# Kernel tuning notes

Hardware: AMD Instinct MI355X
Metric: run time of the kernel (lower is better)

The kernel has to match this reference:

```python
import jax, jax.numpy as jnp
import numpy as np

NUM_HEADS = 6
DIM = 192
WIN = 7  # window_size = (7, 7), n = 49
N = WIN * WIN
TABLE = (2 * WIN - 1) * (2 * WIN - 1)  # 169
SCALE = (DIM // NUM_HEADS) ** (-0.5)


def setup_inputs() -> dict:
    key = jax.random.key(0)
    k1, k2, k3, k4, k5, k6 = jax.random.split(key, 6)
    B_ = 8192   # num_windows * batch = 1024 * 8
    NW = 1024   # windows per image (224/7)^2
    qkv = jax.random.normal(k1, (B_, N, 3 * DIM), dtype=jnp.float32)
    rpi = jax.random.randint(k2, (N, N), 0, TABLE, dtype=jnp.int64)
    # shift-window mask: 0 where attend, -100 where masked (Swin convention)
    mask = jnp.where(jax.random.uniform(k3, (NW, N, N)) < 0.8, 0.0, -100.0).astype(jnp.float32)
    bias_table = 0.02 * jax.random.normal(k4, (TABLE, NUM_HEADS), dtype=jnp.float32)
    proj_w = 0.02 * jax.random.normal(k5, (DIM, DIM), dtype=jnp.float32)
    proj_b = jnp.zeros((DIM,), dtype=jnp.float32)
    return {"qkv": qkv, "rpi": rpi, "mask": mask,
            "bias_table": bias_table, "proj_w": proj_w, "proj_b": proj_b}


def reference(qkv, rpi, mask, bias_table, proj_w, proj_b):
    b_, n, c3 = qkv.shape
    c = c3 // 3
    hd = c // NUM_HEADS
    # (b_, n, 3, h, hd) -> (3, b_, h, n, hd)
    qkv = qkv.reshape(b_, n, 3, NUM_HEADS, hd).transpose(2, 0, 3, 1, 4)
    q, k, v = qkv[0], qkv[1], qkv[2]
    attn = jnp.einsum('bhid,bhjd->bhij', q * SCALE, k)  # (b_, h, n, n)
    # relative position bias gather: (n*n,) -> (n, n, h) -> (h, n, n)
    rpb = bias_table[rpi.reshape(-1)].reshape(n, n, NUM_HEADS).transpose(2, 0, 1)
    attn = attn + rpb[None]
    nw = mask.shape[0]
    attn = attn.reshape(b_ // nw, nw, NUM_HEADS, n, n) + mask[None, :, None]
    attn = jax.nn.softmax(attn.reshape(b_, NUM_HEADS, n, n), axis=-1)
    x = jnp.einsum('bhij,bhjd->bhid', attn, v)          # (b_, h, n, hd)
    x = x.transpose(0, 2, 1, 3).reshape(b_, n, c)
    return x @ proj_w.T + proj_b
```

## Files before the change

### kernel.cpp

```cpp
#include <hip/hip_runtime.h>

#define NH 6
#define NTOK 49
#define CDIM 192
#define NWIN 1024
#define SCALE 0.17677669529663687f

typedef __bf16 bf16x8 __attribute__((ext_vector_type(8)));
typedef float f32x4 __attribute__((ext_vector_type(4)));
typedef unsigned short u16;
typedef unsigned int u32;

__device__ __forceinline__ u16 bfr(float x) { return __builtin_bit_cast(u16, (__bf16)x); }

__global__ void build_wb(const float* __restrict__ w, u16* __restrict__ wb) {
    int i = blockIdx.x * 256 + threadIdx.x;
    if (i < CDIM * CDIM) wb[i] = bfr(w[i]);
}

__global__ __launch_bounds__(256, 4)
void swin_fused(const float* __restrict__ qkv, const int* __restrict__ rpi,
                const float* __restrict__ mask, const float* __restrict__ bias_table,
                const u16* __restrict__ wb, const float* __restrict__ proj_b,
                float* __restrict__ out) {
    __shared__ u16 k_s[64][40];
    __shared__ u16 vT_s[32][72];
    __shared__ u16 p_s[64][72];

    const int tid = threadIdx.x;
    const int b = blockIdx.x;
    const int wn = b & (NWIN - 1);
    const int wv = tid >> 6;
    const int lane = tid & 63;
    const int lg = lane >> 4;
    const int lc = lane & 15;

    const float* qkvb = qkv + (size_t)b * (NTOK * 3 * CDIM);
    const float* mrow = mask + (size_t)wn * (NTOK * NTOK);
    const f32x4 fzero = {0.f, 0.f, 0.f, 0.f};

    const int n0 = tid >> 3, f0 = tid & 7;
    const bool s1 = tid < 136;
    const int n1 = (tid + 256) >> 3, f1 = (tid + 256) & 7;
    const float* kb0 = qkvb + n0 * 576 + CDIM + f0 * 4;
    const float* vb0 = qkvb + n0 * 576 + 2 * CDIM + f0 * 4;
    const float* kb1 = qkvb + n1 * 576 + CDIM + f1 * 4;
    const float* vb1 = qkvb + n1 * 576 + 2 * CDIM + f1 * 4;

    const int qrow = (16 * wv + lc < NTOK) ? 16 * wv + lc : NTOK - 1;
    const float* qptr = qkvb + (size_t)qrow * 576 + 8 * lg;

    float4 kp0 = *reinterpret_cast<const float4*>(kb0);
    float4 vp0 = *reinterpret_cast<const float4*>(vb0);
    float4 kp1 = {0, 0, 0, 0}, vp1 = {0, 0, 0, 0};
    if (s1) {
        kp1 = *reinterpret_cast<const float4*>(kb1);
        vp1 = *reinterpret_cast<const float4*>(vb1);
    }
    float4 qfA = *reinterpret_cast<const float4*>(qptr);
    float4 qfB = *reinterpret_cast<const float4*>(qptr + 4);

    int bofs[4][4];
    float maddf[4][4];
    {
        const int i = 16 * wv + lc;
#pragma unroll
        for (int t = 0; t < 4; ++t)
#pragma unroll
            for (int r = 0; r < 4; ++r) {
                const int j = 16 * t + 4 * lg + r;
                const bool valid = (i < NTOK) && (j < NTOK);
                const int ij = valid ? i * NTOK + j : 0;
                bofs[t][r] = rpi[ij] * NH;
                maddf[t][r] = valid ? mrow[ij] : -1e30f;
            }
    }

    for (int idx = tid; idx < 512; idx += 256) {
        const int d = idx >> 4, m = idx & 15;
        if (m) vT_s[d][48 + m] = 0;
    }
    for (int idx = tid; idx < 600; idx += 256) {
        const int rr = idx / 40, cc = idx % 40;
        k_s[49 + rr][cc] = 0;
    }

    {
        ushort4 ko;
        ko.x = bfr(kp0.x); ko.y = bfr(kp0.y); ko.z = bfr(kp0.z); ko.w = bfr(kp0.w);
        *reinterpret_cast<ushort4*>(&k_s[n0][f0 * 4]) = ko;
        const int d0 = f0 * 4;
        vT_s[d0 + 0][n0] = bfr(vp0.x); vT_s[d0 + 1][n0] = bfr(vp0.y);
        vT_s[d0 + 2][n0] = bfr(vp0.z); vT_s[d0 + 3][n0] = bfr(vp0.w);
        if (s1) {
            ushort4 k1;
            k1.x = bfr(kp1.x); k1.y = bfr(kp1.y); k1.z = bfr(kp1.z); k1.w = bfr(kp1.w);
            *reinterpret_cast<ushort4*>(&k_s[n1][f1 * 4]) = k1;
            const int d1 = f1 * 4;
            vT_s[d1 + 0][n1] = bfr(vp1.x); vT_s[d1 + 1][n1] = bfr(vp1.y);
            vT_s[d1 + 2][n1] = bfr(vp1.z); vT_s[d1 + 3][n1] = bfr(vp1.w);
        }
    }
    __syncthreads();

    bf16x8 af[NH];

#pragma unroll
    for (int h = 0; h < NH; ++h) {
        if (h + 1 < NH) {
            kp0 = *reinterpret_cast<const float4*>(kb0 + (h + 1) * 32);
            vp0 = *reinterpret_cast<const float4*>(vb0 + (h + 1) * 32);
            if (s1) {
                kp1 = *reinterpret_cast<const float4*>(kb1 + (h + 1) * 32);
                vp1 = *reinterpret_cast<const float4*>(vb1 + (h + 1) * 32);
            }
        }

        bf16x8 aq;
        aq[0] = (__bf16)(qfA.x * SCALE); aq[1] = (__bf16)(qfA.y * SCALE);
        aq[2] = (__bf16)(qfA.z * SCALE); aq[3] = (__bf16)(qfA.w * SCALE);
        aq[4] = (__bf16)(qfB.x * SCALE); aq[5] = (__bf16)(qfB.y * SCALE);
        aq[6] = (__bf16)(qfB.z * SCALE); aq[7] = (__bf16)(qfB.w * SCALE);
        if (h + 1 < NH) {
            qfA = *reinterpret_cast<const float4*>(qptr + (h + 1) * 32);
            qfB = *reinterpret_cast<const float4*>(qptr + (h + 1) * 32 + 4);
        }

        float bias_v[4][4];
#pragma unroll
        for (int t = 0; t < 4; ++t)
#pragma unroll
            for (int r = 0; r < 4; ++r)
                bias_v[t][r] = bias_table[bofs[t][r] + h];

        bf16x8 bk[4];
#pragma unroll
        for (int t = 0; t < 4; ++t)
            bk[t] = *reinterpret_cast<const bf16x8*>(&k_s[16 * t + lc][8 * lg]);
        f32x4 acc[4];
#pragma unroll
        for (int t = 0; t < 4; ++t)
            acc[t] = __builtin_amdgcn_mfma_f32_16x16x32_bf16(bk[t], aq, fzero, 0, 0, 0);

        float vals[4][4];
#pragma unroll
        for (int t = 0; t < 4; ++t)
#pragma unroll
            for (int r = 0; r < 4; ++r)
                vals[t][r] = acc[t][r] + bias_v[t][r] + maddf[t][r];

        float mx[4];
#pragma unroll
        for (int t = 0; t < 4; ++t)
            mx[t] = fmaxf(fmaxf(vals[t][0], vals[t][1]), fmaxf(vals[t][2], vals[t][3]));
        float m = fmaxf(fmaxf(mx[0], mx[1]), fmaxf(mx[2], mx[3]));
        m = fmaxf(m, __shfl_xor(m, 16));
        m = fmaxf(m, __shfl_xor(m, 32));

        float e[4][4];
        float s = 0.f;
#pragma unroll
        for (int t = 0; t < 4; ++t) {
            float st = 0.f;
#pragma unroll
            for (int r = 0; r < 4; ++r) { e[t][r] = __expf(vals[t][r] - m); st += e[t][r]; }
            s += st;
        }
        s += __shfl_xor(s, 16);
        s += __shfl_xor(s, 32);
        const float rs = 1.0f / s;

        {
            u16* prow = &p_s[16 * wv + lc][4 * lg];
#pragma unroll
            for (int t = 0; t < 4; ++t) {
                ushort4 pk;
                pk.x = bfr(e[t][0] * rs); pk.y = bfr(e[t][1] * rs);
                pk.z = bfr(e[t][2] * rs); pk.w = bfr(e[t][3] * rs);
                *reinterpret_cast<ushort4*>(prow + 16 * t) = pk;
            }
        }

        f32x4 xacc[2] = {fzero, fzero};
#pragma unroll
        for (int ks = 0; ks < 2; ++ks) {
            const bf16x8 pa = *reinterpret_cast<const bf16x8*>(&p_s[16 * wv + lc][32 * ks + 8 * lg]);
#pragma unroll
            for (int ct = 0; ct < 2; ++ct) {
                const bf16x8 vv = *reinterpret_cast<const bf16x8*>(&vT_s[16 * ct + lc][32 * ks + 8 * lg]);
                xacc[ct] = __builtin_amdgcn_mfma_f32_16x16x32_bf16(pa, vv, xacc[ct], 0, 0, 0);
            }
        }

#pragma unroll
        for (int ct = 0; ct < 2; ++ct)
#pragma unroll
            for (int r = 0; r < 4; ++r)
                p_s[16 * wv + 4 * lg + r][16 * ct + lc] = bfr(xacc[ct][r]);
        af[h] = *reinterpret_cast<const bf16x8*>(&p_s[16 * wv + lc][8 * lg]);

        if (h + 1 < NH) {
            __syncthreads();
            ushort4 ko;
            ko.x = bfr(kp0.x); ko.y = bfr(kp0.y); ko.z = bfr(kp0.z); ko.w = bfr(kp0.w);
            *reinterpret_cast<ushort4*>(&k_s[n0][f0 * 4]) = ko;
            const int d0 = f0 * 4;
            vT_s[d0 + 0][n0] = bfr(vp0.x); vT_s[d0 + 1][n0] = bfr(vp0.y);
            vT_s[d0 + 2][n0] = bfr(vp0.z); vT_s[d0 + 3][n0] = bfr(vp0.w);
            if (s1) {
                ushort4 k1;
                k1.x = bfr(kp1.x); k1.y = bfr(kp1.y); k1.z = bfr(kp1.z); k1.w = bfr(kp1.w);
                *reinterpret_cast<ushort4*>(&k_s[n1][f1 * 4]) = k1;
                const int d1 = f1 * 4;
                vT_s[d1 + 0][n1] = bfr(vp1.x); vT_s[d1 + 1][n1] = bfr(vp1.y);
                vT_s[d1 + 2][n1] = bfr(vp1.z); vT_s[d1 + 3][n1] = bfr(vp1.w);
            }
            __syncthreads();
        }
    }

    f32x4 pacc[12];
#pragma unroll
    for (int ct = 0; ct < 12; ++ct) pacc[ct] = fzero;

#pragma unroll
    for (int ks = 0; ks < NH; ++ks) {
#pragma unroll
        for (int ct = 0; ct < 12; ++ct) {
            const bf16x8 bw = *reinterpret_cast<const bf16x8*>(wb + (16 * ct + lc) * CDIM + ks * 32 + 8 * lg);
            pacc[ct] = __builtin_amdgcn_mfma_f32_16x16x32_bf16(af[ks], bw, pacc[ct], 0, 0, 0);
        }
    }

#pragma unroll
    for (int ct = 0; ct < 12; ++ct) {
        const int c = 16 * ct + lc;
        const float pb = proj_b[c];
#pragma unroll
        for (int r = 0; r < 4; ++r) {
            const int i = 16 * wv + 4 * lg + r;
            if (i < NTOK)
                out[(size_t)b * (NTOK * CDIM) + i * CDIM + c] = pacc[ct][r] + pb;
        }
    }
}

extern "C" void kernel_launch(void* const* d_in, const int* in_sizes, int n_in,
                              void* d_out, int out_size, void* d_ws, size_t ws_size,
                              hipStream_t stream) {
    const float* qkv        = (const float*)d_in[0];
    const int*   rpi        = (const int*)d_in[1];
    const float* mask       = (const float*)d_in[2];
    const float* bias_table = (const float*)d_in[3];
    const float* proj_w     = (const float*)d_in[4];
    const float* proj_b     = (const float*)d_in[5];
    float* out = (float*)d_out;
    u16* wb = (u16*)d_ws;

    const int nblk = in_sizes[0] / (NTOK * 3 * CDIM);

    build_wb<<<(CDIM * CDIM + 255) / 256, 256, 0, stream>>>(proj_w, wb);
    swin_fused<<<nblk, 256, 0, stream>>>(qkv, rpi, mask, bias_table, wb, proj_b, out);
}
```

Measured before the change: 561.4 us.

## Load K/V per wave directly from global and split projection by output columns

Each wave now reads its own K and V fragments straight from global memory into registers in MFMA layout, so the shared K/V staging buffers and the two block barriers per head go away. Per-head attention outputs go to a shared row buffer, and after one barrier each wave computes 48 output columns for all 64 rows of the projection instead of all 192 columns for its 16 rows. The cost is that every wave loads all of K and V, which is four times the global and L2 traffic for those, and the V loads are scalar strided reads that are poorly coalesced.

```diff
diff --git a/kernel.cpp b/kernel.cpp
--- a/kernel.cpp
+++ b/kernel.cpp
@@ -23,9 +23,8 @@
                 const float* __restrict__ mask, const float* __restrict__ bias_table,
                 const u16* __restrict__ wb, const float* __restrict__ proj_b,
                 float* __restrict__ out) {
-    __shared__ u16 k_s[64][40];
-    __shared__ u16 vT_s[32][72];
-    __shared__ u16 p_s[64][72];
+    __shared__ u16 xb_s[64][200];
+    __shared__ u16 p_s[4][16][72];
 
     const int tid = threadIdx.x;
     const int b = blockIdx.x;
@@ -39,24 +38,26 @@
     const float* mrow = mask + (size_t)wn * (NTOK * NTOK);
     const f32x4 fzero = {0.f, 0.f, 0.f, 0.f};
 
-    const int n0 = tid >> 3, f0 = tid & 7;
-    const bool s1 = tid < 136;
-    const int n1 = (tid + 256) >> 3, f1 = (tid + 256) & 7;
-    const float* kb0 = qkvb + n0 * 576 + CDIM + f0 * 4;
-    const float* vb0 = qkvb + n0 * 576 + 2 * CDIM + f0 * 4;
-    const float* kb1 = qkvb + n1 * 576 + CDIM + f1 * 4;
-    const float* vb1 = qkvb + n1 * 576 + 2 * CDIM + f1 * 4;
-
     const int qrow = (16 * wv + lc < NTOK) ? 16 * wv + lc : NTOK - 1;
     const float* qptr = qkvb + (size_t)qrow * 576 + 8 * lg;
-
-    float4 kp0 = *reinterpret_cast<const float4*>(kb0);
-    float4 vp0 = *reinterpret_cast<const float4*>(vb0);
-    float4 kp1 = {0, 0, 0, 0}, vp1 = {0, 0, 0, 0};
-    if (s1) {
-        kp1 = *reinterpret_cast<const float4*>(kb1);
-        vp1 = *reinterpret_cast<const float4*>(vb1);
-    }
+    const float* kptr[4];
+#pragma unroll
+    for (int t = 0; t < 4; ++t) {
+        const int krow = (16 * t + lc < NTOK) ? 16 * t + lc : NTOK - 1;
+        kptr[t] = qkvb + (size_t)krow * 576 + CDIM + 8 * lg;
+    }
+    const float* vptr[2];
+    int vrow[2][8];
+#pragma unroll
+    for (int ks = 0; ks < 2; ++ks)
+#pragma unroll
+        for (int j = 0; j < 8; ++j) {
+            const int r = 32 * ks + 8 * lg + j;
+            vrow[ks][j] = (r < NTOK ? r : NTOK - 1) * 576;
+        }
+    vptr[0] = qkvb + 2 * CDIM + lc;
+    vptr[1] = qkvb + 2 * CDIM + lc;
+
     float4 qfA = *reinterpret_cast<const float4*>(qptr);
     float4 qfB = *reinterpret_cast<const float4*>(qptr + 4);
 
@@ -76,45 +77,29 @@
             }
     }
 
-    for (int idx = tid; idx < 512; idx += 256) {
-        const int d = idx >> 4, m = idx & 15;
-        if (m) vT_s[d][48 + m] = 0;
-    }
-    for (int idx = tid; idx < 600; idx += 256) {
-        const int rr = idx / 40, cc = idx % 40;
-        k_s[49 + rr][cc] = 0;
-    }
-
-    {
-        ushort4 ko;
-        ko.x = bfr(kp0.x); ko.y = bfr(kp0.y); ko.z = bfr(kp0.z); ko.w = bfr(kp0.w);
-        *reinterpret_cast<ushort4*>(&k_s[n0][f0 * 4]) = ko;
-        const int d0 = f0 * 4;
-        vT_s[d0 + 0][n0] = bfr(vp0.x); vT_s[d0 + 1][n0] = bfr(vp0.y);
-        vT_s[d0 + 2][n0] = bfr(vp0.z); vT_s[d0 + 3][n0] = bfr(vp0.w);
-        if (s1) {
-            ushort4 k1;
-            k1.x = bfr(kp1.x); k1.y = bfr(kp1.y); k1.z = bfr(kp1.z); k1.w = bfr(kp1.w);
-            *reinterpret_cast<ushort4*>(&k_s[n1][f1 * 4]) = k1;
-            const int d1 = f1 * 4;
-            vT_s[d1 + 0][n1] = bfr(vp1.x); vT_s[d1 + 1][n1] = bfr(vp1.y);
-            vT_s[d1 + 2][n1] = bfr(vp1.z); vT_s[d1 + 3][n1] = bfr(vp1.w);
-        }
-    }
-    __syncthreads();
-
-    bf16x8 af[NH];
-
 #pragma unroll
     for (int h = 0; h < NH; ++h) {
-        if (h + 1 < NH) {
-            kp0 = *reinterpret_cast<const float4*>(kb0 + (h + 1) * 32);
-            vp0 = *reinterpret_cast<const float4*>(vb0 + (h + 1) * 32);
-            if (s1) {
-                kp1 = *reinterpret_cast<const float4*>(kb1 + (h + 1) * 32);
-                vp1 = *reinterpret_cast<const float4*>(vb1 + (h + 1) * 32);
-            }
-        }
+        float4 kfA[4], kfB[4];
+#pragma unroll
+        for (int t = 0; t < 4; ++t) {
+            kfA[t] = *reinterpret_cast<const float4*>(kptr[t] + h * 32);
+            kfB[t] = *reinterpret_cast<const float4*>(kptr[t] + h * 32 + 4);
+        }
+        float vf[2][2][8];
+#pragma unroll
+        for (int ct = 0; ct < 2; ++ct)
+#pragma unroll
+            for (int ks = 0; ks < 2; ++ks)
+#pragma unroll
+                for (int j = 0; j < 8; ++j)
+                    vf[ct][ks][j] = vptr[ks][vrow[ks][j] + h * 32 + 16 * ct];
+
+        float bias_v[4][4];
+#pragma unroll
+        for (int t = 0; t < 4; ++t)
+#pragma unroll
+            for (int r = 0; r < 4; ++r)
+                bias_v[t][r] = bias_table[bofs[t][r] + h];
 
         bf16x8 aq;
         aq[0] = (__bf16)(qfA.x * SCALE); aq[1] = (__bf16)(qfA.y * SCALE);
@@ -126,21 +111,16 @@
             qfB = *reinterpret_cast<const float4*>(qptr + (h + 1) * 32 + 4);
         }
 
-        float bias_v[4][4];
-#pragma unroll
-        for (int t = 0; t < 4; ++t)
-#pragma unroll
-            for (int r = 0; r < 4; ++r)
-                bias_v[t][r] = bias_table[bofs[t][r] + h];
-
-        bf16x8 bk[4];
-#pragma unroll
-        for (int t = 0; t < 4; ++t)
-            bk[t] = *reinterpret_cast<const bf16x8*>(&k_s[16 * t + lc][8 * lg]);
         f32x4 acc[4];
 #pragma unroll
-        for (int t = 0; t < 4; ++t)
-            acc[t] = __builtin_amdgcn_mfma_f32_16x16x32_bf16(bk[t], aq, fzero, 0, 0, 0);
+        for (int t = 0; t < 4; ++t) {
+            bf16x8 bk;
+            bk[0] = (__bf16)kfA[t].x; bk[1] = (__bf16)kfA[t].y;
+            bk[2] = (__bf16)kfA[t].z; bk[3] = (__bf16)kfA[t].w;
+            bk[4] = (__bf16)kfB[t].x; bk[5] = (__bf16)kfB[t].y;
+            bk[6] = (__bf16)kfB[t].z; bk[7] = (__bf16)kfB[t].w;
+            acc[t] = __builtin_amdgcn_mfma_f32_16x16x32_bf16(bk, aq, fzero, 0, 0, 0);
+        }
 
         float vals[4][4];
 #pragma unroll
@@ -171,7 +151,7 @@
         const float rs = 1.0f / s;
 
         {
-            u16* prow = &p_s[16 * wv + lc][4 * lg];
+            u16* prow = &p_s[wv][lc][4 * lg];
 #pragma unroll
             for (int t = 0; t < 4; ++t) {
                 ushort4 pk;
@@ -181,66 +161,67 @@
             }
         }
 
+        bf16x8 vv[2][2];
+#pragma unroll
+        for (int ct = 0; ct < 2; ++ct)
+#pragma unroll
+            for (int ks = 0; ks < 2; ++ks)
+#pragma unroll
+                for (int j = 0; j < 8; ++j)
+                    vv[ct][ks][j] = (__bf16)vf[ct][ks][j];
+
         f32x4 xacc[2] = {fzero, fzero};
 #pragma unroll
         for (int ks = 0; ks < 2; ++ks) {
-            const bf16x8 pa = *reinterpret_cast<const bf16x8*>(&p_s[16 * wv + lc][32 * ks + 8 * lg]);
-#pragma unroll
-            for (int ct = 0; ct < 2; ++ct) {
-                const bf16x8 vv = *reinterpret_cast<const bf16x8*>(&vT_s[16 * ct + lc][32 * ks + 8 * lg]);
-                xacc[ct] = __builtin_amdgcn_mfma_f32_16x16x32_bf16(pa, vv, xacc[ct], 0, 0, 0);
+            const bf16x8 pa = *reinterpret_cast<const bf16x8*>(&p_s[wv][lc][32 * ks + 8 * lg]);
+#pragma unroll
+            for (int ct = 0; ct < 2; ++ct)
+                xacc[ct] = __builtin_amdgcn_mfma_f32_16x16x32_bf16(pa, vv[ct][ks], xacc[ct], 0, 0, 0);
+        }
+
+#pragma unroll
+        for (int ct = 0; ct < 2; ++ct)
+#pragma unroll
+            for (int r = 0; r < 4; ++r)
+                xb_s[16 * wv + 4 * lg + r][32 * h + 16 * ct + lc] = bfr(xacc[ct][r]);
+    }
+
+    __syncthreads();
+
+    f32x4 pacc[3][4];
+#pragma unroll
+    for (int ct = 0; ct < 3; ++ct)
+#pragma unroll
+        for (int rt = 0; rt < 4; ++rt) pacc[ct][rt] = fzero;
+
+#pragma unroll
+    for (int ks = 0; ks < 6; ++ks) {
+        bf16x8 af[4];
+#pragma unroll
+        for (int rt = 0; rt < 4; ++rt)
+            af[rt] = *reinterpret_cast<const bf16x8*>(&xb_s[16 * rt + lc][32 * ks + 8 * lg]);
+#pragma unroll
+        for (int ct = 0; ct < 3; ++ct) {
+            const int c = 48 * wv + 16 * ct + lc;
+            const bf16x8 bw = *reinterpret_cast<const bf16x8*>(wb + c * CDIM + 32 * ks + 8 * lg);
+#pragma unroll
+            for (int rt = 0; rt < 4; ++rt)
+                pacc[ct][rt] = __builtin_amdgcn_mfma_f32_16x16x32_bf16(af[rt], bw, pacc[ct][rt], 0, 0, 0);
+        }
+    }
+
+#pragma unroll
+    for (int ct = 0; ct < 3; ++ct) {
+        const int c = 48 * wv + 16 * ct + lc;
+        const float pb = proj_b[c];
+#pragma unroll
+        for (int rt = 0; rt < 4; ++rt) {
+#pragma unroll
+            for (int r = 0; r < 4; ++r) {
+                const int i = 16 * rt + 4 * lg + r;
+                if (i < NTOK)
+                    out[(size_t)b * (NTOK * CDIM) + i * CDIM + c] = pacc[ct][rt][r] + pb;
             }
-        }
-
-#pragma unroll
-        for (int ct = 0; ct < 2; ++ct)
-#pragma unroll
-            for (int r = 0; r < 4; ++r)
-                p_s[16 * wv + 4 * lg + r][16 * ct + lc] = bfr(xacc[ct][r]);
-        af[h] = *reinterpret_cast<const bf16x8*>(&p_s[16 * wv + lc][8 * lg]);
-
-        if (h + 1 < NH) {
-            __syncthreads();
-            ushort4 ko;
-            ko.x = bfr(kp0.x); ko.y = bfr(kp0.y); ko.z = bfr(kp0.z); ko.w = bfr(kp0.w);
-            *reinterpret_cast<ushort4*>(&k_s[n0][f0 * 4]) = ko;
-            const int d0 = f0 * 4;
-            vT_s[d0 + 0][n0] = bfr(vp0.x); vT_s[d0 + 1][n0] = bfr(vp0.y);
-            vT_s[d0 + 2][n0] = bfr(vp0.z); vT_s[d0 + 3][n0] = bfr(vp0.w);
-            if (s1) {
-                ushort4 k1;
-                k1.x = bfr(kp1.x); k1.y = bfr(kp1.y); k1.z = bfr(kp1.z); k1.w = bfr(kp1.w);
-                *reinterpret_cast<ushort4*>(&k_s[n1][f1 * 4]) = k1;
-                const int d1 = f1 * 4;
-                vT_s[d1 + 0][n1] = bfr(vp1.x); vT_s[d1 + 1][n1] = bfr(vp1.y);
-                vT_s[d1 + 2][n1] = bfr(vp1.z); vT_s[d1 + 3][n1] = bfr(vp1.w);
-            }
-            __syncthreads();
-        }
-    }
-
-    f32x4 pacc[12];
-#pragma unroll
-    for (int ct = 0; ct < 12; ++ct) pacc[ct] = fzero;
-
-#pragma unroll
-    for (int ks = 0; ks < NH; ++ks) {
-#pragma unroll
-        for (int ct = 0; ct < 12; ++ct) {
-            const bf16x8 bw = *reinterpret_cast<const bf16x8*>(wb + (16 * ct + lc) * CDIM + ks * 32 + 8 * lg);
-            pacc[ct] = __builtin_amdgcn_mfma_f32_16x16x32_bf16(af[ks], bw, pacc[ct], 0, 0, 0);
-        }
-    }
-
-#pragma unroll
-    for (int ct = 0; ct < 12; ++ct) {
-        const int c = 16 * ct + lc;
-        const float pb = proj_b[c];
-#pragma unroll
-        for (int r = 0; r < 4; ++r) {
-            const int i = 16 * wv + 4 * lg + r;
-            if (i < NTOK)
-                out[(size_t)b * (NTOK * CDIM) + i * CDIM + c] = pacc[ct][r] + pb;
         }
     }
 }
```

After: 891.9 us. 1.59x slower.
